# Kernel tuning notes

Hardware: AMD Instinct MI355X
Metric: run time of the kernel (lower is better)

## Reference

```python
import jax, jax.numpy as jnp
import numpy as np


def setup_inputs() -> dict:
    key = jax.random.key(0)
    k = jax.random.split(key, 4)
    B, D, H, W, C = 4, 64, 64, 64, 64
    R = 16  # reduction ratio
    KS = 7
    x = jax.random.normal(k[0], (B, D, H, W, C), dtype=jnp.float32)
    w1 = jax.random.normal(k[1], (C, C // R), dtype=jnp.float32) * (2.0 / C) ** 0.5
    b1 = jnp.zeros((C // R,), dtype=jnp.float32)
    w2 = jax.random.normal(k[2], (C // R, C), dtype=jnp.float32) * (2.0 / (C // R)) ** 0.5
    b2 = jnp.zeros((C,), dtype=jnp.float32)
    conv_w = jax.random.normal(k[3], (KS, KS, KS, 2, 1), dtype=jnp.float32) * (2.0 / (KS ** 3 * 2)) ** 0.5
    return {"x": x, "w1": w1, "b1": b1, "w2": w2, "b2": b2, "conv_w": conv_w}


def _mlp(v, w1, b1, w2, b2):
    # shared two-layer MLP: relu then sigmoid
    h = jax.nn.relu(v @ w1 + b1)
    return jax.nn.sigmoid(h @ w2 + b2)


def reference(x, w1, b1, w2, b2, conv_w):
    # ---- channel attention ----
    avg_pool = jnp.mean(x, axis=(1, 2, 3))          # [B, C]
    max_pool = jnp.max(x, axis=(1, 2, 3))           # [B, C]
    ca = _mlp(avg_pool, w1, b1, w2, b2) + _mlp(max_pool, w1, b1, w2, b2)  # [B, C]
    channel_refined = x * ca[:, None, None, None, :]  # [B, D, H, W, C]
    # ---- spatial attention ----
    avg_sp = jnp.mean(channel_refined, axis=-1, keepdims=True)  # [B,D,H,W,1]
    max_sp = jnp.max(channel_refined, axis=-1, keepdims=True)   # [B,D,H,W,1]
    concat = jnp.concatenate([avg_sp, max_sp], axis=-1)          # [B,D,H,W,2]
    sa = jax.lax.conv_general_dilated(
        concat, conv_w,
        window_strides=(1, 1, 1), padding="SAME",
        dimension_numbers=("NDHWC", "DHWIO", "NDHWC"),
    )  # [B,D,H,W,1]
    sa = jax.nn.sigmoid(sa)
    return channel_refined * sa
```

## Files before the change

### kernel.cpp

```cpp
#include <hip/hip_runtime.h>
#include <hip/hip_fp16.h>
#include <math.h>

#define BATCH 4
#define SPATIAL (64*64*64)
#define NB 512

typedef float f32x4 __attribute__((ext_vector_type(4)));
typedef unsigned int u32x4 __attribute__((ext_vector_type(4)));

__device__ __forceinline__ float sigmoidf_(float z) { return 1.f / (1.f + expf(-z)); }

template<bool W16>
__global__ __launch_bounds__(256) void pool_partial_kernel(
    const float* __restrict__ x, __half* __restrict__ x16,
    float* __restrict__ psum, float* __restrict__ pmax) {
  const int b     = blockIdx.x / NB;
  const int chunk = blockIdx.x % NB;
  const int tid  = threadIdx.x;
  const int w    = tid >> 6;
  const int lane = tid & 63;
  const int q    = lane >> 4;
  const int g    = lane & 15;

  const f32x4* xb = (const f32x4*)x + (size_t)b * SPATIAL * 16;
  uint2* x16b = (uint2*)x16 + (size_t)b * SPATIAL * 16;

  float s0=0.f, s1=0.f, s2=0.f, s3=0.f;
  float m0=-INFINITY, m1=-INFINITY, m2=-INFINITY, m3=-INFINITY;

  const int PPB = SPATIAL / NB;
  #pragma unroll 8
  for (int i = 0; i < PPB / 16; ++i) {
    int p = chunk * PPB + i * 16 + w * 4 + q;
    size_t gi = (size_t)p * 16 + g;
    f32x4 v;
    if (W16) v = __builtin_nontemporal_load(xb + gi);
    else     v = xb[gi];
    if (W16) {
      union { __half2 h[2]; uint2 u; } pk;
      pk.h[0] = __floats2half2_rn(v.x, v.y);
      pk.h[1] = __floats2half2_rn(v.z, v.w);
      x16b[gi] = pk.u;
    }
    s0 += v.x; s1 += v.y; s2 += v.z; s3 += v.w;
    m0 = fmaxf(m0, v.x); m1 = fmaxf(m1, v.y); m2 = fmaxf(m2, v.z); m3 = fmaxf(m3, v.w);
  }
  #pragma unroll
  for (int mask = 16; mask <= 32; mask <<= 1) {
    s0 += __shfl_xor(s0, mask); s1 += __shfl_xor(s1, mask);
    s2 += __shfl_xor(s2, mask); s3 += __shfl_xor(s3, mask);
    m0 = fmaxf(m0, __shfl_xor(m0, mask)); m1 = fmaxf(m1, __shfl_xor(m1, mask));
    m2 = fmaxf(m2, __shfl_xor(m2, mask)); m3 = fmaxf(m3, __shfl_xor(m3, mask));
  }
  __shared__ float lsum[4][64];
  __shared__ float lmax[4][64];
  if (q == 0) {
    lsum[w][g*4+0] = s0; lsum[w][g*4+1] = s1; lsum[w][g*4+2] = s2; lsum[w][g*4+3] = s3;
    lmax[w][g*4+0] = m0; lmax[w][g*4+1] = m1; lmax[w][g*4+2] = m2; lmax[w][g*4+3] = m3;
  }
  __syncthreads();
  if (tid < 64) {
    float s = lsum[0][tid] + lsum[1][tid] + lsum[2][tid] + lsum[3][tid];
    float m = fmaxf(fmaxf(lmax[0][tid], lmax[1][tid]), fmaxf(lmax[2][tid], lmax[3][tid]));
    psum[((size_t)b * 64 + tid) * NB + chunk] = s;
    pmax[((size_t)b * 64 + tid) * NB + chunk] = m;
  }
}

__global__ __launch_bounds__(256) void ca_kernel(
    const float* __restrict__ psum, const float* __restrict__ pmax,
    const float* __restrict__ w1, const float* __restrict__ b1,
    const float* __restrict__ w2, const float* __restrict__ b2,
    const float* __restrict__ cw, __half2* __restrict__ w16,
    float* __restrict__ ca) {
  const int b = blockIdx.x;
  const int tid = threadIdx.x;
  for (int wi = tid; wi < 343; wi += 256)
    w16[wi] = __floats2half2_rn(cw[wi * 2], cw[wi * 2 + 1]);

  const int r = tid >> 6, c = tid & 63;
  const f32x4* ps4 = (const f32x4*)(psum + ((size_t)b * 64 + c) * NB + r * 128);
  const f32x4* pm4 = (const f32x4*)(pmax + ((size_t)b * 64 + c) * NB + r * 128);
  float s = 0.f, m = -INFINITY;
  #pragma unroll 8
  for (int j = 0; j < 32; ++j) {
    f32x4 vs = ps4[j];
    f32x4 vm = pm4[j];
    s += (vs.x + vs.y) + (vs.z + vs.w);
    m = fmaxf(m, fmaxf(fmaxf(vm.x, vm.y), fmaxf(vm.z, vm.w)));
  }
  __shared__ float ls[4][64];
  __shared__ float lm[4][64];
  ls[r][c] = s; lm[r][c] = m;
  __syncthreads();
  if (tid < 64) {
    const int cc = tid;
    float ss = ls[0][cc] + ls[1][cc] + ls[2][cc] + ls[3][cc];
    float mm = fmaxf(fmaxf(lm[0][cc], lm[1][cc]), fmaxf(lm[2][cc], lm[3][cc]));
    float avg = ss * (1.f / SPATIAL);

    float w1c[4];
    #pragma unroll
    for (int j = 0; j < 4; ++j) w1c[j] = w1[cc * 4 + j];
    float pa[4], pm[4];
    #pragma unroll
    for (int j = 0; j < 4; ++j) { pa[j] = avg * w1c[j]; pm[j] = mm * w1c[j]; }
    #pragma unroll
    for (int mask = 1; mask < 64; mask <<= 1) {
      #pragma unroll
      for (int j = 0; j < 4; ++j) {
        pa[j] += __shfl_xor(pa[j], mask);
        pm[j] += __shfl_xor(pm[j], mask);
      }
    }
    float za = b2[cc], zm = b2[cc];
    #pragma unroll
    for (int j = 0; j < 4; ++j) {
      float ha = fmaxf(pa[j] + b1[j], 0.f);
      float hm = fmaxf(pm[j] + b1[j], 0.f);
      za += ha * w2[j * 64 + cc];
      zm += hm * w2[j * 64 + cc];
    }
    ca[b * 64 + cc] = sigmoidf_(za) + sigmoidf_(zm);
  }
}

__global__ __launch_bounds__(256) void spstats16_kernel(
    const __half* __restrict__ x16, const float* __restrict__ ca, __half2* __restrict__ sp) {
  const int tid = threadIdx.x, lane = tid & 63, w = tid >> 6;
  const int q = lane >> 3, g = lane & 7;
  const int waveId = blockIdx.x * 4 + w;
  const int nWaves = gridDim.x * 4;
  const int NGRP = BATCH * SPATIAL / 8;
  const u32x4* x4 = (const u32x4*)x16;
  for (int grp = waveId; grp < NGRP; grp += nWaves) {
    int p = grp * 8 + q;
    int b = p >> 18;
    union { u32x4 v; unsigned u[4]; } uu;
    uu.v = x4[(size_t)p * 8 + g];
    const float* cab = ca + b * 64 + g * 8;
    f32x4 c0 = *(const f32x4*)cab;
    f32x4 c1 = *(const f32x4*)(cab + 4);
    float2 f0 = __half22float2(*(__half2*)&uu.u[0]);
    float2 f1 = __half22float2(*(__half2*)&uu.u[1]);
    float2 f2 = __half22float2(*(__half2*)&uu.u[2]);
    float2 f3 = __half22float2(*(__half2*)&uu.u[3]);
    float a0 = f0.x*c0.x, a1 = f0.y*c0.y, a2 = f1.x*c0.z, a3 = f1.y*c0.w;
    float a4 = f2.x*c1.x, a5 = f2.y*c1.y, a6 = f3.x*c1.z, a7 = f3.y*c1.w;
    float s = ((a0+a1)+(a2+a3)) + ((a4+a5)+(a6+a7));
    float m = fmaxf(fmaxf(fmaxf(a0,a1),fmaxf(a2,a3)), fmaxf(fmaxf(a4,a5),fmaxf(a6,a7)));
    #pragma unroll
    for (int mask = 1; mask < 8; mask <<= 1) {
      s += __shfl_xor(s, mask);
      m = fmaxf(m, __shfl_xor(m, mask));
    }
    if (g == 0) sp[p] = __floats2half2_rn(s * (1.f / 64.f), m);
  }
}

__global__ __launch_bounds__(256) void spstats_kernel(
    const float* __restrict__ x, const float* __restrict__ ca, __half2* __restrict__ sp) {
  const int tid = threadIdx.x, lane = tid & 63, w = tid >> 6;
  const int q = lane >> 4, g = lane & 15;
  const int waveId = blockIdx.x * 4 + w;
  const int nWaves = gridDim.x * 4;
  const int NGRP = BATCH * SPATIAL / 4;
  const float4* x4  = (const float4*)x;
  const float4* ca4 = (const float4*)ca;
  for (int grp = waveId; grp < NGRP; grp += nWaves) {
    int p = grp * 4 + q;
    int b = p >> 18;
    float4 v  = x4[(size_t)p * 16 + g];
    float4 cv = ca4[b * 16 + g];
    float ax = v.x * cv.x, ay = v.y * cv.y, az = v.z * cv.z, aw = v.w * cv.w;
    float s = ax + ay + az + aw;
    float m = fmaxf(fmaxf(ax, ay), fmaxf(az, aw));
    #pragma unroll
    for (int mask = 1; mask < 16; mask <<= 1) {
      s += __shfl_xor(s, mask);
      m = fmaxf(m, __shfl_xor(m, mask));
    }
    if (g == 0) sp[p] = __floats2half2_rn(s * (1.f / 64.f), m);
  }
}

#define CZT 8
#define CYT 2
#define CPL (CZT + 6)
#define CRW (CYT + 6)
#define CXW 70
template<bool X16>
__global__ __launch_bounds__(256) void conv_final_kernel(
    const __half2* __restrict__ sp, const __half2* __restrict__ w16,
    const float* __restrict__ x, const __half* __restrict__ x16,
    const float* __restrict__ ca, float* __restrict__ out) {
  __shared__ __half2 tile[CPL * CRW * CXW];

  const int bid = blockIdx.x;
  const int zg = bid & 7;
  const int yg = (bid >> 3) & 31;
  const int b  = bid >> 8;
  const int z0 = zg * CZT;
  const int y0 = yg * CYT;

  const __half2* spb = sp + (size_t)b * SPATIAL;

  const int NE = CPL * CRW * CXW;
  for (int e = threadIdx.x; e < NE; e += 256) {
    int pl  = e / (CRW * CXW);
    int rem = e - pl * (CRW * CXW);
    int row = rem / CXW;
    int xi  = rem - row * CXW;
    int z = z0 + pl - 3;
    int y = y0 + row - 3;
    int xx = xi - 3;
    __half2 v = __floats2half2_rn(0.f, 0.f);
    if ((unsigned)z < 64u && (unsigned)y < 64u && (unsigned)xx < 64u)
      v = spb[(z << 12) + (y << 6) + xx];
    tile[e] = v;
  }
  __syncthreads();

  const int lane = threadIdx.x & 63;
  const int ty   = threadIdx.x >> 6;
  const int zb   = ty * 2;

  float accf[2][2] = {{0.f, 0.f}, {0.f, 0.f}};

  const __half2 zero2 = __floats2half2_rn(0.f, 0.f);
  for (int pp = 0; pp < 8; ++pp) {
    const int pl = zb + pp;
    __half2 a00 = zero2, a01 = zero2, a10 = zero2, a11 = zero2;
    #pragma unroll
    for (int ry = 0; ry < 8; ++ry) {
      const __half2* rowp = tile + (pl * CRW + ry) * CXW + lane;
      __half2 h[7];
      #pragma unroll
      for (int k = 0; k < 7; ++k) h[k] = rowp[k];
      #pragma unroll
      for (int dz = 0; dz < 2; ++dz) {
        const int kz = pp - dz;
        if ((unsigned)kz > 6u) continue;
        #pragma unroll
        for (int dy = 0; dy < 2; ++dy) {
          const int ky = ry - dy;
          if ((unsigned)ky > 6u) continue;
          const __half2* wp = w16 + kz * 49 + ky * 7;
          __half2 a = (dz == 0) ? (dy == 0 ? a00 : a01) : (dy == 0 ? a10 : a11);
          #pragma unroll
          for (int kx = 0; kx < 7; ++kx)
            a = __hfma2(h[kx], wp[kx], a);
          if (dz == 0) { if (dy == 0) a00 = a; else a01 = a; }
          else         { if (dy == 0) a10 = a; else a11 = a; }
        }
      }
    }
    accf[0][0] += __low2float(a00) + __high2float(a00);
    accf[0][1] += __low2float(a01) + __high2float(a01);
    accf[1][0] += __low2float(a10) + __high2float(a10);
    accf[1][1] += __low2float(a11) + __high2float(a11);
  }

  if (X16) {
    const float4* ca4 = (const float4*)ca;
    const float4 cav = ca4[b * 16 + (lane & 15)];
    const uint2* xr = (const uint2*)x16;
    #pragma unroll
    for (int dz = 0; dz < 2; ++dz) {
      #pragma unroll
      for (int dy = 0; dy < 2; ++dy) {
        const float s_own = sigmoidf_(accf[dz][dy]);
        const int z = z0 + zb + dz;
        const int y = y0 + dy;
        const size_t base = (((size_t)b * 64 + z) * 64 + y) * 1024;
        #pragma unroll 8
        for (int k = 0; k < 16; ++k) {
          const int f = lane + k * 64;
          const float sv = __shfl(s_own, (lane >> 4) + k * 4);
          uint2 u = xr[base + f];
          float2 t0 = __half22float2(*(__half2*)&u.x);
          float2 t1 = __half22float2(*(__half2*)&u.y);
          f32x4 o;
          o.x = t0.x * cav.x * sv; o.y = t0.y * cav.y * sv;
          o.z = t1.x * cav.z * sv; o.w = t1.y * cav.w * sv;
          __builtin_nontemporal_store(o, (f32x4*)out + base + f);
        }
      }
    }
  } else {
    const float4* x4 = (const float4*)x;
    const float4* ca4 = (const float4*)ca;
    const float4 cav = ca4[b * 16 + (lane & 15)];
    #pragma unroll
    for (int dz = 0; dz < 2; ++dz) {
      #pragma unroll
      for (int dy = 0; dy < 2; ++dy) {
        const float s_own = sigmoidf_(accf[dz][dy]);
        const int z = z0 + zb + dz;
        const int y = y0 + dy;
        const size_t base = (((size_t)b * 64 + z) * 64 + y) * 1024;
        #pragma unroll 8
        for (int k = 0; k < 16; ++k) {
          const int f = lane + k * 64;
          const float sv = __shfl(s_own, (lane >> 4) + k * 4);
          float4 v = x4[base + f];
          f32x4 o;
          o.x = v.x * cav.x * sv; o.y = v.y * cav.y * sv;
          o.z = v.z * cav.z * sv; o.w = v.w * cav.w * sv;
          __builtin_nontemporal_store(o, (f32x4*)(out + (base + f) * 4));
        }
      }
    }
  }
}

extern "C" void kernel_launch(void* const* d_in, const int* in_sizes, int n_in,
                              void* d_out, int out_size, void* d_ws, size_t ws_size,
                              hipStream_t stream) {
  const float* x  = (const float*)d_in[0];
  const float* w1 = (const float*)d_in[1];
  const float* b1 = (const float*)d_in[2];
  const float* w2 = (const float*)d_in[3];
  const float* b2 = (const float*)d_in[4];
  const float* cw = (const float*)d_in[5];
  float* out = (float*)d_out;

  const size_t x16_bytes = (size_t)BATCH * SPATIAL * 64 * 2;
  const size_t sp_bytes  = (size_t)BATCH * SPATIAL * 4;
  const size_t red_bytes = (size_t)BATCH * NB * 64 * 4;
  const size_t tail_bytes = 256 * 4 + 344 * 4 + 1024;
  const size_t need = x16_bytes + sp_bytes + 2 * red_bytes + tail_bytes;

  if (ws_size >= need) {
    __half*  x16  = (__half*)d_ws;
    __half2* sp   = (__half2*)((char*)d_ws + x16_bytes);
    float*   psum = (float*)((char*)sp + sp_bytes);
    float*   pmax = psum + (size_t)BATCH * NB * 64;
    float*   ca   = pmax + (size_t)BATCH * NB * 64;
    __half2* w16  = (__half2*)(ca + 256);

    pool_partial_kernel<true><<<BATCH * NB, 256, 0, stream>>>(x, x16, psum, pmax);
    ca_kernel<<<BATCH, 256, 0, stream>>>(psum, pmax, w1, b1, w2, b2, cw, w16, ca);
    spstats16_kernel<<<2048, 256, 0, stream>>>(x16, ca, sp);
    conv_final_kernel<true><<<BATCH * 32 * 8, 256, 0, stream>>>(sp, w16, x, x16, ca, out);
  } else {
    __half2* sp   = (__half2*)d_ws;
    float*   psum = (float*)((char*)sp + sp_bytes);
    float*   pmax = psum + (size_t)BATCH * NB * 64;
    float*   ca   = pmax + (size_t)BATCH * NB * 64;
    __half2* w16  = (__half2*)(ca + 256);

    pool_partial_kernel<false><<<BATCH * NB, 256, 0, stream>>>(x, nullptr, psum, pmax);
    ca_kernel<<<BATCH, 256, 0, stream>>>(psum, pmax, w1, b1, w2, b2, cw, w16, ca);
    spstats_kernel<<<2048, 256, 0, stream>>>(x, ca, sp);
    conv_final_kernel<false><<<BATCH * 32 * 8, 256, 0, stream>>>(sp, w16, x, nullptr, ca, out);
  }
}
```

Before: 182.8 us.

## Use fp32-accumulating dot2 in conv, shrink z-tile, unroll spstats loop

```diff
diff --git a/kernel.cpp b/kernel.cpp
--- a/kernel.cpp
+++ b/kernel.cpp
@@ -8,8 +8,20 @@
 
 typedef float f32x4 __attribute__((ext_vector_type(4)));
 typedef unsigned int u32x4 __attribute__((ext_vector_type(4)));
+typedef _Float16 f16x2 __attribute__((ext_vector_type(2)));
 
 __device__ __forceinline__ float sigmoidf_(float z) { return 1.f / (1.f + expf(-z)); }
+
+__device__ __forceinline__ float dot2acc(__half2 a, __half2 b, float c) {
+#if __has_builtin(__builtin_amdgcn_fdot2)
+  union { __half2 h; f16x2 f; } ua, ub;
+  ua.h = a; ub.h = b;
+  return __builtin_amdgcn_fdot2(ua.f, ub.f, c, false);
+#else
+  float2 fa = __half22float2(a), fb = __half22float2(b);
+  return fmaf(fa.x, fb.x, fmaf(fa.y, fb.y, c));
+#endif
+}
 
 template<bool W16>
 __global__ __launch_bounds__(256) void pool_partial_kernel(
@@ -134,6 +146,7 @@
   const int nWaves = gridDim.x * 4;
   const int NGRP = BATCH * SPATIAL / 8;
   const u32x4* x4 = (const u32x4*)x16;
+  #pragma unroll 2
   for (int grp = waveId; grp < NGRP; grp += nWaves) {
     int p = grp * 8 + q;
     int b = p >> 18;
@@ -185,7 +198,7 @@
   }
 }
 
-#define CZT 8
+#define CZT 4
 #define CYT 2
 #define CPL (CZT + 6)
 #define CRW (CYT + 6)
@@ -198,9 +211,9 @@
   __shared__ __half2 tile[CPL * CRW * CXW];
 
   const int bid = blockIdx.x;
-  const int zg = bid & 7;
-  const int yg = (bid >> 3) & 31;
-  const int b  = bid >> 8;
+  const int zg = bid & 15;
+  const int yg = (bid >> 4) & 31;
+  const int b  = bid >> 9;
   const int z0 = zg * CZT;
   const int y0 = yg * CYT;
 
@@ -224,68 +237,50 @@
 
   const int lane = threadIdx.x & 63;
   const int ty   = threadIdx.x >> 6;
-  const int zb   = ty * 2;
-
-  float accf[2][2] = {{0.f, 0.f}, {0.f, 0.f}};
-
-  const __half2 zero2 = __floats2half2_rn(0.f, 0.f);
-  for (int pp = 0; pp < 8; ++pp) {
-    const int pl = zb + pp;
-    __half2 a00 = zero2, a01 = zero2, a10 = zero2, a11 = zero2;
+
+  float acc0 = 0.f, acc1 = 0.f;
+
+  for (int pp = 0; pp < 7; ++pp) {
+    const int pl = ty + pp;
     #pragma unroll
     for (int ry = 0; ry < 8; ++ry) {
       const __half2* rowp = tile + (pl * CRW + ry) * CXW + lane;
       __half2 h[7];
       #pragma unroll
       for (int k = 0; k < 7; ++k) h[k] = rowp[k];
-      #pragma unroll
-      for (int dz = 0; dz < 2; ++dz) {
-        const int kz = pp - dz;
-        if ((unsigned)kz > 6u) continue;
+      if (ry <= 6) {
+        const __half2* wp = w16 + pp * 49 + ry * 7;
         #pragma unroll
-        for (int dy = 0; dy < 2; ++dy) {
-          const int ky = ry - dy;
-          if ((unsigned)ky > 6u) continue;
-          const __half2* wp = w16 + kz * 49 + ky * 7;
-          __half2 a = (dz == 0) ? (dy == 0 ? a00 : a01) : (dy == 0 ? a10 : a11);
-          #pragma unroll
-          for (int kx = 0; kx < 7; ++kx)
-            a = __hfma2(h[kx], wp[kx], a);
-          if (dz == 0) { if (dy == 0) a00 = a; else a01 = a; }
-          else         { if (dy == 0) a10 = a; else a11 = a; }
-        }
-      }
-    }
-    accf[0][0] += __low2float(a00) + __high2float(a00);
-    accf[0][1] += __low2float(a01) + __high2float(a01);
-    accf[1][0] += __low2float(a10) + __high2float(a10);
-    accf[1][1] += __low2float(a11) + __high2float(a11);
-  }
-
+        for (int kx = 0; kx < 7; ++kx) acc0 = dot2acc(h[kx], wp[kx], acc0);
+      }
+      if (ry >= 1) {
+        const __half2* wp = w16 + pp * 49 + (ry - 1) * 7;
+        #pragma unroll
+        for (int kx = 0; kx < 7; ++kx) acc1 = dot2acc(h[kx], wp[kx], acc1);
+      }
+    }
+  }
+
+  const int z = z0 + ty;
   if (X16) {
     const float4* ca4 = (const float4*)ca;
     const float4 cav = ca4[b * 16 + (lane & 15)];
     const uint2* xr = (const uint2*)x16;
     #pragma unroll
-    for (int dz = 0; dz < 2; ++dz) {
-      #pragma unroll
-      for (int dy = 0; dy < 2; ++dy) {
-        const float s_own = sigmoidf_(accf[dz][dy]);
-        const int z = z0 + zb + dz;
-        const int y = y0 + dy;
-        const size_t base = (((size_t)b * 64 + z) * 64 + y) * 1024;
-        #pragma unroll 8
-        for (int k = 0; k < 16; ++k) {
-          const int f = lane + k * 64;
-          const float sv = __shfl(s_own, (lane >> 4) + k * 4);
-          uint2 u = xr[base + f];
-          float2 t0 = __half22float2(*(__half2*)&u.x);
-          float2 t1 = __half22float2(*(__half2*)&u.y);
-          f32x4 o;
-          o.x = t0.x * cav.x * sv; o.y = t0.y * cav.y * sv;
-          o.z = t1.x * cav.z * sv; o.w = t1.y * cav.w * sv;
-          __builtin_nontemporal_store(o, (f32x4*)out + base + f);
-        }
+    for (int dy = 0; dy < 2; ++dy) {
+      const float s_own = sigmoidf_(dy == 0 ? acc0 : acc1);
+      const size_t base = (((size_t)b * 64 + z) * 64 + (y0 + dy)) * 1024;
+      #pragma unroll 8
+      for (int k = 0; k < 16; ++k) {
+        const int f = lane + k * 64;
+        const float sv = __shfl(s_own, (lane >> 4) + k * 4);
+        uint2 u = xr[base + f];
+        float2 t0 = __half22float2(*(__half2*)&u.x);
+        float2 t1 = __half22float2(*(__half2*)&u.y);
+        f32x4 o;
+        o.x = t0.x * cav.x * sv; o.y = t0.y * cav.y * sv;
+        o.z = t1.x * cav.z * sv; o.w = t1.y * cav.w * sv;
+        __builtin_nontemporal_store(o, (f32x4*)out + base + f);
       }
     }
   } else {
@@ -293,23 +288,18 @@
     const float4* ca4 = (const float4*)ca;
     const float4 cav = ca4[b * 16 + (lane & 15)];
     #pragma unroll
-    for (int dz = 0; dz < 2; ++dz) {
-      #pragma unroll
-      for (int dy = 0; dy < 2; ++dy) {
-        const float s_own = sigmoidf_(accf[dz][dy]);
-        const int z = z0 + zb + dz;
-        const int y = y0 + dy;
-        const size_t base = (((size_t)b * 64 + z) * 64 + y) * 1024;
-        #pragma unroll 8
-        for (int k = 0; k < 16; ++k) {
-          const int f = lane + k * 64;
-          const float sv = __shfl(s_own, (lane >> 4) + k * 4);
-          float4 v = x4[base + f];
-          f32x4 o;
-          o.x = v.x * cav.x * sv; o.y = v.y * cav.y * sv;
-          o.z = v.z * cav.z * sv; o.w = v.w * cav.w * sv;
-          __builtin_nontemporal_store(o, (f32x4*)(out + (base + f) * 4));
-        }
+    for (int dy = 0; dy < 2; ++dy) {
+      const float s_own = sigmoidf_(dy == 0 ? acc0 : acc1);
+      const size_t base = (((size_t)b * 64 + z) * 64 + (y0 + dy)) * 1024;
+      #pragma unroll 8
+      for (int k = 0; k < 16; ++k) {
+        const int f = lane + k * 64;
+        const float sv = __shfl(s_own, (lane >> 4) + k * 4);
+        float4 v = x4[base + f];
+        f32x4 o;
+        o.x = v.x * cav.x * sv; o.y = v.y * cav.y * sv;
+        o.z = v.z * cav.z * sv; o.w = v.w * cav.w * sv;
+        __builtin_nontemporal_store(o, (f32x4*)(out + (base + f) * 4));
       }
     }
   }
@@ -332,6 +322,8 @@
   const size_t tail_bytes = 256 * 4 + 344 * 4 + 1024;
   const size_t need = x16_bytes + sp_bytes + 2 * red_bytes + tail_bytes;
 
+  const int conv_grid = BATCH * 16 * 32;
+
   if (ws_size >= need) {
     __half*  x16  = (__half*)d_ws;
     __half2* sp   = (__half2*)((char*)d_ws + x16_bytes);
@@ -343,7 +335,7 @@
     pool_partial_kernel<true><<<BATCH * NB, 256, 0, stream>>>(x, x16, psum, pmax);
     ca_kernel<<<BATCH, 256, 0, stream>>>(psum, pmax, w1, b1, w2, b2, cw, w16, ca);
     spstats16_kernel<<<2048, 256, 0, stream>>>(x16, ca, sp);
-    conv_final_kernel<true><<<BATCH * 32 * 8, 256, 0, stream>>>(sp, w16, x, x16, ca, out);
+    conv_final_kernel<true><<<conv_grid, 256, 0, stream>>>(sp, w16, x, x16, ca, out);
   } else {
     __half2* sp   = (__half2*)d_ws;
     float*   psum = (float*)((char*)sp + sp_bytes);
@@ -354,6 +346,6 @@
     pool_partial_kernel<false><<<BATCH * NB, 256, 0, stream>>>(x, nullptr, psum, pmax);
     ca_kernel<<<BATCH, 256, 0, stream>>>(psum, pmax, w1, b1, w2, b2, cw, w16, ca);
     spstats_kernel<<<2048, 256, 0, stream>>>(x, ca, sp);
-    conv_final_kernel<false><<<BATCH * 32 * 8, 256, 0, stream>>>(sp, w16, x, nullptr, ca, out);
-  }
-}
+    conv_final_kernel<false><<<conv_grid, 256, 0, stream>>>(sp, w16, x, nullptr, ca, out);
+  }
+}
```

Result: no change. 183.5 us (+0.4%).
